# Kernel optimization log

Measured on AMD Instinct MI355X. Metric: run time of the kernel, lower is better.

The kernel has to match this reference:

```python
import jax, jax.numpy as jnp
import numpy as np

NUM_ITERS = 20
TAU = 1.0
NEG_BIG = -1e9


def setup_inputs() -> dict:
    key = jax.random.key(0)
    k1, k2 = jax.random.split(key)
    B, S, V = 8, 512, 32000
    predictions = jax.random.normal(k1, (B, S, V), dtype=jnp.float32)
    targets = jax.random.randint(k2, (B, S), 0, V, dtype=jnp.int64)
    return {"predictions": predictions, "targets": targets}


def reference(predictions, targets):
    B, S, V = predictions.shape
    # per-token cross entropy (reduction='none'): lse(logits) - logit[target]
    lse = jax.scipy.special.logsumexp(predictions, axis=-1)            # (B, S)
    tgt_logit = jnp.take_along_axis(predictions, targets[..., None], axis=-1)[..., 0]
    ce = lse - tgt_logit                                               # (B, S)
    # torch code: ce.view(B, S, -1) -> (B, S, 1)
    ce3 = ce[..., None]                                                # (B, S, 1)
    cost = -ce3 / TAU                                                  # (B, S, 1)
    if S < V:
        # faithful to torch: pad last dim (size 1) by V - S -> width V - S + 1
        cost = jnp.pad(cost, ((0, 0), (0, 0), (0, V - S)), constant_values=NEG_BIG)
    elif S > V:
        cost = cost[:, :, :V]

    def body(c, _):
        c = c - jax.scipy.special.logsumexp(c, axis=2, keepdims=True)
        c = c - jax.scipy.special.logsumexp(c, axis=1, keepdims=True)
        return c, None

    cost, _ = jax.lax.scan(body, cost, None, length=NUM_ITERS)
    matching = jnp.exp(cost)                                           # (B, S, W)
    loss = jnp.sum(matching * ce3, axis=(1, 2)).mean()
    return loss
```

## Files before the change

kernel.cpp:

```cpp
#include <hip/hip_runtime.h>
#include <math.h>

#define BATCH     8
#define SEQ       512
#define VOCAB     32000
#define PADCOLS   31488.0f
#define NEG_BIG   (-1000000000.0f)
#define NUM_ITERS 20

__global__ __launch_bounds__(256) void ce_kernel(const float* __restrict__ pred,
                                                 const int*   __restrict__ tgt,
                                                 float*       __restrict__ ce) {
    const int row = blockIdx.x;
    const float* __restrict__ p = pred + (size_t)row * VOCAB;
    const int tid = threadIdx.x;

    float m0 = -INFINITY, m1 = -INFINITY, m2 = -INFINITY, m3 = -INFINITY;
    float s0 = 0.0f, s1 = 0.0f, s2 = 0.0f, s3 = 0.0f;

    const float4* __restrict__ p4 = (const float4*)p;
    for (int i = tid; i < VOCAB / 4; i += 256) {
        float4 v = p4[i];
        float n0 = fmaxf(m0, v.x); s0 = s0 * __expf(m0 - n0) + __expf(v.x - n0); m0 = n0;
        float n1 = fmaxf(m1, v.y); s1 = s1 * __expf(m1 - n1) + __expf(v.y - n1); m1 = n1;
        float n2 = fmaxf(m2, v.z); s2 = s2 * __expf(m2 - n2) + __expf(v.z - n2); m2 = n2;
        float n3 = fmaxf(m3, v.w); s3 = s3 * __expf(m3 - n3) + __expf(v.w - n3); m3 = n3;
    }

    float m = fmaxf(fmaxf(m0, m1), fmaxf(m2, m3));
    float s = s0 * __expf(m0 - m) + s1 * __expf(m1 - m)
            + s2 * __expf(m2 - m) + s3 * __expf(m3 - m);

    #pragma unroll
    for (int off = 1; off < 64; off <<= 1) {
        float mo = __shfl_xor(m, off);
        float so = __shfl_xor(s, off);
        float mn = fmaxf(m, mo);
        s = s * __expf(m - mn) + so * __expf(mo - mn);
        m = mn;
    }

    __shared__ float sm[4], ss[4];
    if ((tid & 63) == 0) { sm[tid >> 6] = m; ss[tid >> 6] = s; }
    __syncthreads();
    if (tid == 0) {
        float M = sm[0], S = ss[0];
        #pragma unroll
        for (int w = 1; w < 4; ++w) {
            float mo = sm[w], so = ss[w];
            float mn = fmaxf(M, mo);
            S = S * __expf(M - mn) + so * __expf(mo - mn);
            M = mn;
        }
        float lse = M + logf(S);
        ce[row] = lse - p[tgt[row]];
    }
}

__global__ __launch_bounds__(512) void sinkhorn_kernel(const float* __restrict__ ce,
                                                       float*       __restrict__ out) {
    const int tid  = threadIdx.x;
    const int b    = tid >> 6;
    const int lane = tid & 63;

    float u[8], r[8], c[8];
    #pragma unroll
    for (int j = 0; j < 8; ++j) {
        c[j] = ce[b * SEQ + j * 64 + lane];
        u[j] = -c[j];
        r[j] = NEG_BIG;
    }

    for (int it = 0; it < NUM_ITERS; ++it) {
        #pragma unroll
        for (int j = 0; j < 8; ++j) {
            float m   = fmaxf(u[j], r[j]);
            float sum = expf(u[j] - m) + PADCOLS * expf(r[j] - m);
            float L2  = m + logf(sum);
            u[j] -= L2;
            r[j] -= L2;
        }
        {
            float m = u[0];
            #pragma unroll
            for (int j = 1; j < 8; ++j) m = fmaxf(m, u[j]);
            #pragma unroll
            for (int off = 1; off < 64; off <<= 1) m = fmaxf(m, __shfl_xor(m, off));
            float s = 0.0f;
            #pragma unroll
            for (int j = 0; j < 8; ++j) s += expf(u[j] - m);
            #pragma unroll
            for (int off = 1; off < 64; off <<= 1) s += __shfl_xor(s, off);
            float L1 = m + logf(s);
            #pragma unroll
            for (int j = 0; j < 8; ++j) u[j] -= L1;
        }
        {
            float m = r[0];
            #pragma unroll
            for (int j = 1; j < 8; ++j) m = fmaxf(m, r[j]);
            #pragma unroll
            for (int off = 1; off < 64; off <<= 1) m = fmaxf(m, __shfl_xor(m, off));
            float s = 0.0f;
            #pragma unroll
            for (int j = 0; j < 8; ++j) s += expf(r[j] - m);
            #pragma unroll
            for (int off = 1; off < 64; off <<= 1) s += __shfl_xor(s, off);
            float L1 = m + logf(s);
            #pragma unroll
            for (int j = 0; j < 8; ++j) r[j] -= L1;
        }
    }

    float acc = 0.0f;
    #pragma unroll
    for (int j = 0; j < 8; ++j)
        acc += (expf(u[j]) + PADCOLS * expf(r[j])) * c[j];
    #pragma unroll
    for (int off = 1; off < 64; off <<= 1) acc += __shfl_xor(acc, off);

    __shared__ float part[8];
    if (lane == 0) part[b] = acc;
    __syncthreads();
    if (tid == 0) {
        float t = 0.0f;
        #pragma unroll
        for (int w = 0; w < 8; ++w) t += part[w];
        out[0] = t / (float)BATCH;
    }
}

extern "C" void kernel_launch(void* const* d_in, const int* in_sizes, int n_in,
                              void* d_out, int out_size, void* d_ws, size_t ws_size,
                              hipStream_t stream) {
    const float* pred = (const float*)d_in[0];
    const int*   tgt  = (const int*)d_in[1];
    float* out = (float*)d_out;
    float* ce  = (float*)d_ws;

    ce_kernel<<<BATCH * SEQ, 256, 0, stream>>>(pred, tgt, ce);
    sinkhorn_kernel<<<1, 512, 0, stream>>>(ce, out);
}
```

Measured before the change: 717.8 us.

## Map one wavefront per CE row and cut online-softmax rescaling exps

```diff
diff --git a/kernel.cpp b/kernel.cpp
--- a/kernel.cpp
+++ b/kernel.cpp
@@ -11,25 +11,35 @@
 __global__ __launch_bounds__(256) void ce_kernel(const float* __restrict__ pred,
                                                  const int*   __restrict__ tgt,
                                                  float*       __restrict__ ce) {
-    const int row = blockIdx.x;
-    const float* __restrict__ p = pred + (size_t)row * VOCAB;
-    const int tid = threadIdx.x;
+    const int tid  = threadIdx.x;
+    const int lane = tid & 63;
+    const int row  = (blockIdx.x << 2) + (tid >> 6);
+    const float4* __restrict__ p4 = (const float4*)(pred + (size_t)row * VOCAB);
 
-    float m0 = -INFINITY, m1 = -INFINITY, m2 = -INFINITY, m3 = -INFINITY;
-    float s0 = 0.0f, s1 = 0.0f, s2 = 0.0f, s3 = 0.0f;
+    float m0 = -INFINITY, s0 = 0.0f;
+    float m1 = -INFINITY, s1 = 0.0f;
 
-    const float4* __restrict__ p4 = (const float4*)p;
-    for (int i = tid; i < VOCAB / 4; i += 256) {
-        float4 v = p4[i];
-        float n0 = fmaxf(m0, v.x); s0 = s0 * __expf(m0 - n0) + __expf(v.x - n0); m0 = n0;
-        float n1 = fmaxf(m1, v.y); s1 = s1 * __expf(m1 - n1) + __expf(v.y - n1); m1 = n1;
-        float n2 = fmaxf(m2, v.z); s2 = s2 * __expf(m2 - n2) + __expf(v.z - n2); m2 = n2;
-        float n3 = fmaxf(m3, v.w); s3 = s3 * __expf(m3 - n3) + __expf(v.w - n3); m3 = n3;
+    #pragma unroll 5
+    for (int k = 0; k < 125; ++k) {
+        float4 v = p4[lane + (k << 6)];
+        float lm = fmaxf(fmaxf(v.x, v.y), fmaxf(v.z, v.w));
+        if (k & 1) {
+            float nm = fmaxf(m1, lm);
+            s1 = s1 * __expf(m1 - nm)
+               + ((__expf(v.x - nm) + __expf(v.y - nm))
+                + (__expf(v.z - nm) + __expf(v.w - nm)));
+            m1 = nm;
+        } else {
+            float nm = fmaxf(m0, lm);
+            s0 = s0 * __expf(m0 - nm)
+               + ((__expf(v.x - nm) + __expf(v.y - nm))
+                + (__expf(v.z - nm) + __expf(v.w - nm)));
+            m0 = nm;
+        }
     }
 
-    float m = fmaxf(fmaxf(m0, m1), fmaxf(m2, m3));
-    float s = s0 * __expf(m0 - m) + s1 * __expf(m1 - m)
-            + s2 * __expf(m2 - m) + s3 * __expf(m3 - m);
+    float m = fmaxf(m0, m1);
+    float s = s0 * __expf(m0 - m) + s1 * __expf(m1 - m);
 
     #pragma unroll
     for (int off = 1; off < 64; off <<= 1) {
@@ -40,20 +50,9 @@
         m = mn;
     }
 
-    __shared__ float sm[4], ss[4];
-    if ((tid & 63) == 0) { sm[tid >> 6] = m; ss[tid >> 6] = s; }
-    __syncthreads();
-    if (tid == 0) {
-        float M = sm[0], S = ss[0];
-        #pragma unroll
-        for (int w = 1; w < 4; ++w) {
-            float mo = sm[w], so = ss[w];
-            float mn = fmaxf(M, mo);
-            S = S * __expf(M - mn) + so * __expf(mo - mn);
-            M = mn;
-        }
-        float lse = M + logf(S);
-        ce[row] = lse - p[tgt[row]];
+    if (lane == 0) {
+        float lse = m + logf(s);
+        ce[row] = lse - pred[(size_t)row * VOCAB + tgt[row]];
     }
 }
 
@@ -138,6 +137,6 @@
     float* out = (float*)d_out;
     float* ce  = (float*)d_ws;
 
-    ce_kernel<<<BATCH * SEQ, 256, 0, stream>>>(pred, tgt, ce);
+    ce_kernel<<<(BATCH * SEQ) / 4, 256, 0, stream>>>(pred, tgt, ce);
     sinkhorn_kernel<<<1, 512, 0, stream>>>(ce, out);
 }
```

New measurement: 722.7 us. No clear change (+0.7%).
